# Kernel optimization log

Measured on AMD Instinct MI355X. Metric: run time of the kernel, lower is better.

Reference implementation:

```python
import jax, jax.numpy as jnp
import numpy as np

EMBED = 1024
HEADS = 16
HEAD_DIM = EMBED // HEADS


def setup_inputs() -> dict:
    key = jax.random.key(0)
    k1, k2, k3, k4, k5 = jax.random.split(key, 5)
    N, S = 2, 2048
    values = jax.random.normal(k1, (N, S, EMBED), dtype=jnp.float32)
    keys = jax.random.normal(k2, (N, S, EMBED), dtype=jnp.float32)
    query = jax.random.normal(k3, (N, S, EMBED), dtype=jnp.float32)
    mask = jnp.ones((N, 1, S, S), dtype=jnp.int32)
    # fc_out: Linear(heads*head_dim, embed_size) with bias; torch stores W as [out, in]
    W_out = jax.random.normal(k4, (EMBED, EMBED), dtype=jnp.float32) / np.sqrt(EMBED)
    b_out = jax.random.normal(k5, (EMBED,), dtype=jnp.float32) * 0.01
    return {"values": values, "keys": keys, "query": query, "mask": mask,
            "W_out": W_out, "b_out": b_out}


def reference(values, keys, query, mask, W_out, b_out):
    N, S, E = query.shape
    H, D = HEADS, HEAD_DIM
    # NOTE: source module never applies its q/k/v Linear layers (bug preserved).
    v = values.reshape(N, S, H, D)
    k = keys.reshape(N, S, H, D)
    q = query.reshape(N, S, H, D)
    energy = jnp.einsum('nqhd,nkhd->nhqk', q, k)  # [N,H,S,S]
    energy = jnp.where(mask == 0, jnp.float32(-1e20), energy)
    # non-standard scale: sqrt(embed_size), faithful to source
    attn = jax.nn.softmax(energy / jnp.sqrt(jnp.float32(E)), axis=3)
    out = jnp.einsum('nhql,nlhd->nqhd', attn, v).reshape(N, S, H * D)
    return out @ W_out.T + b_out
```

## Files before the change

### kernel.cpp

```cpp
#include <hip/hip_runtime.h>
#include <stdint.h>

#define S_LEN 2048
#define EMB 1024
#define NHEADS 16
#define HD 64
#define LOG2E 1.4426950408889634f
#define NROWS 65536

typedef __bf16 bf16x8 __attribute__((ext_vector_type(8)));
typedef float f32x4 __attribute__((ext_vector_type(4)));
typedef unsigned short u16;

#define MFMA16(a, b, c) __builtin_amdgcn_mfma_f32_16x16x32_bf16(a, b, c, 0, 0, 0)
#define GLOAD_LDS16(gp, lp)                                        \
  __builtin_amdgcn_global_load_lds(                                \
      (const __attribute__((address_space(1))) unsigned int*)(gp), \
      (__attribute__((address_space(3))) unsigned int*)(lp), 16, 0, 0)

__device__ __forceinline__ u16 bf16r(float x) {
  union { float f; unsigned int u; } c; c.f = x;
  unsigned int u = c.u + 0x7fffu + ((c.u >> 16) & 1u);
  return (u16)(u >> 16);
}

__device__ __forceinline__ unsigned int cvt_pk_bf16(float lo, float hi) {
  unsigned int r;
  asm("v_cvt_pk_bf16_f32 %0, %1, %2" : "=v"(r) : "v"(lo), "v"(hi));
  return r;
}

__device__ __forceinline__ float fexp2(float x) {
  float r;
  asm("v_exp_f32 %0, %1" : "=v"(r) : "v"(x));
  return r;
}

__device__ __forceinline__ float fmax3(float a, float b, float c) {
  float r;
  asm("v_max3_f32 %0, %1, %2, %3" : "=v"(r) : "v"(a), "v"(b), "v"(c));
  return r;
}

__device__ __forceinline__ float bf_lo(unsigned int v) {
  union { unsigned int u; float f; } c; c.u = v << 16; return c.f;
}
__device__ __forceinline__ float bf_hi(unsigned int v) {
  union { unsigned int u; float f; } c; c.u = v & 0xffff0000u; return c.f;
}

__device__ __forceinline__ int kperm(int k) {
  int kb = (k >> 4) & 3, g = (k >> 2) & 3, r = k & 3;
  return (kb >> 1) * 32 + g * 8 + (kb & 1) * 4 + r;
}

__global__ __launch_bounds__(256) void prep_kernel(
    const float* __restrict__ values, const float* __restrict__ keys,
    const float* __restrict__ W, const int* __restrict__ mask,
    u16* __restrict__ vt, u16* __restrict__ kb, u16* __restrict__ wb,
    unsigned char* __restrict__ fl2) {
  __shared__ u16 tile[64][65];
  __shared__ int s_ok[4];
  int b = blockIdx.x;
  int t = threadIdx.x;
  if (b < 1024) {
    int st = b & 31, h = (b >> 5) & 15, n = b >> 9;
    int s0 = st * 64;
    int d = t & 63, r4 = t >> 6;
#pragma unroll
    for (int i = 0; i < 16; ++i) {
      int s = r4 + i * 4;
      float x = values[(size_t)(n * S_LEN + s0 + s) * EMB + h * HD + d];
      tile[s][d] = bf16r(x);
    }
    __syncthreads();
    int sp = s0 + kperm(d);
#pragma unroll
    for (int i = 0; i < 16; ++i) {
      int dd = r4 + i * 4;
      vt[(size_t)((n * NHEADS + h) * HD + dd) * S_LEN + sp] = tile[d][dd];
    }
  } else if (b < 2048) {
    int idx = (b - 1024) * 256 + t;
    const float4* in4 = (const float4*)keys;
    ushort4* out4 = (ushort4*)kb;
#pragma unroll
    for (int j = 0; j < 4; ++j) {
      float4 v = in4[idx + j * 262144];
      ushort4 o;
      o.x = bf16r(v.x); o.y = bf16r(v.y); o.z = bf16r(v.z); o.w = bf16r(v.w);
      out4[idx + j * 262144] = o;
    }
  } else if (b < 2304) {
    int idx = (b - 2048) * 256 + t;
    const float4* in4 = (const float4*)W;
    ushort4* out4 = (ushort4*)wb;
#pragma unroll
    for (int j = 0; j < 4; ++j) {
      float4 v = in4[idx + j * 65536];
      ushort4 o;
      o.x = bf16r(v.x); o.y = bf16r(v.y); o.z = bf16r(v.z); o.w = bf16r(v.w);
      out4[idx + j * 65536] = o;
    }
  } else {
    int idx = b - 2304;
    int kt = idx & 31, qt = (idx >> 5) & 15, n = idx >> 9;
    int qr = t >> 1, c8 = t & 1;
    const int4* mp = (const int4*)(mask + (size_t)n * S_LEN * S_LEN +
                                   (size_t)(qt * 128 + qr) * S_LEN + kt * 64) + c8 * 8;
    int ok = 1;
#pragma unroll
    for (int i = 0; i < 8; ++i) {
      int4 m = mp[i];
      ok &= (m.x != 0) & (m.y != 0) & (m.z != 0) & (m.w != 0);
    }
    ok = __all(ok);
    if ((t & 63) == 0) s_ok[t >> 6] = ok;
    __syncthreads();
    if (t == 0) fl2[idx] = (unsigned char)(s_ok[0] & s_ok[1] & s_ok[2] & s_ok[3]);
  }
}

__global__ __launch_bounds__(256, 4) void attn_kernel(
    const float* __restrict__ query, const u16* __restrict__ kbuf,
    const u16* __restrict__ vt, const int* __restrict__ mask,
    const unsigned char* __restrict__ fl2, u16* __restrict__ po,
    float2* __restrict__ ml) {
  __shared__ __align__(16) unsigned char kl[2][8192];
  __shared__ __align__(16) unsigned char vl[2][8192];

  int b = blockIdx.x;
  b = (b & 7) * 128 + (b >> 3);
  int qt = b & 15, half = (b >> 4) & 1, h = (b >> 5) & 15, n = b >> 9;
  int t = threadIdx.x, w = t >> 6, l = t & 63, l16 = l & 15, g = l >> 4;
  int q0 = qt * 128 + w * 32;
  int kt0 = half * 16;

  const float QS = 0.03125f * LOG2E;
  bf16x8 aq[2][2];
#pragma unroll
  for (int u = 0; u < 2; ++u)
#pragma unroll
    for (int hh = 0; hh < 2; ++hh) {
      const float* qp = query + (size_t)(n * S_LEN + q0 + u * 16 + l16) * EMB +
                        h * HD + hh * 32 + g * 8;
      float4 f0 = *(const float4*)qp;
      float4 f1 = *(const float4*)(qp + 4);
      union { bf16x8 v; unsigned int u32[4]; } qq;
      qq.u32[0] = cvt_pk_bf16(f0.x * QS, f0.y * QS);
      qq.u32[1] = cvt_pk_bf16(f0.z * QS, f0.w * QS);
      qq.u32[2] = cvt_pk_bf16(f1.x * QS, f1.y * QS);
      qq.u32[3] = cvt_pk_bf16(f1.z * QS, f1.w * QS);
      aq[u][hh] = qq.v;
    }

  union { bf16x8 v; unsigned int u32[4]; } one_i;
  one_i.u32[0] = 0x3F803F80u; one_i.u32[1] = 0x3F803F80u;
  one_i.u32[2] = 0x3F803F80u; one_i.u32[3] = 0x3F803F80u;
  bf16x8 ones = one_i.v;

  f32x4 zero4 = {0.f, 0.f, 0.f, 0.f};
  f32x4 acc[2][4];
  float lrun[2] = {0.f, 0.f}, mrun[2] = {0.f, 0.f};
#pragma unroll
  for (int u = 0; u < 2; ++u)
#pragma unroll
    for (int db = 0; db < 4; ++db) acc[u][db] = zero4;

  int row_s = t >> 3, cc = t & 7;
  int sc = cc ^ (row_s & 7);
  const u16* gk0 = kbuf + (size_t)(n * S_LEN + row_s) * EMB + h * HD + sc * 8;
  const u16* gv0 = vt + (size_t)((n * NHEADS + h) * HD + row_s) * S_LEN + sc * 8;

  auto stage = [&](int kt, int nb) {
    const u16* gk = gk0 + (size_t)kt * 64 * EMB;
    const u16* gv = gv0 + kt * 64;
    GLOAD_LDS16(gk, kl[nb] + (w * 64) * 16);
    GLOAD_LDS16(gk + 32 * EMB, kl[nb] + (256 + w * 64) * 16);
    GLOAD_LDS16(gv, vl[nb] + (w * 64) * 16);
    GLOAD_LDS16(gv + 32 * S_LEN, vl[nb] + (256 + w * 64) * 16);
  };

  auto body = [&](int kt, const unsigned char* kc, const unsigned char* vc) {
    f32x4 sf[2][4];
    __builtin_amdgcn_s_setprio(1);
#pragma unroll
    for (int kb = 0; kb < 4; ++kb) {
      int row = kb * 16 + l16;
      const unsigned char* kr = kc + row * 128;
      int sw = (row & 7) << 4;
      bf16x8 bk0 = *(const bf16x8*)(kr + ((g * 16) ^ sw));
      bf16x8 bk1 = *(const bf16x8*)(kr + ((64 + g * 16) ^ sw));
#pragma unroll
      for (int u = 0; u < 2; ++u) {
        f32x4 z = zero4;
        z = MFMA16(bk0, aq[u][0], z);
        z = MFMA16(bk1, aq[u][1], z);
        sf[u][kb] = z;
      }
    }
    __builtin_amdgcn_s_setprio(0);

    unsigned char fflag = fl2[((n * 16 + qt) * 32) + kt];
    if (!fflag) {
#pragma unroll
      for (int u = 0; u < 2; ++u) {
        const int* mrow = mask + (size_t)n * S_LEN * S_LEN +
                          (size_t)(q0 + u * 16 + l16) * S_LEN + kt * 64 + g * 4;
#pragma unroll
        for (int kb = 0; kb < 4; ++kb) {
          int4 mm = *(const int4*)(mrow + kb * 16);
          if (mm.x == 0) sf[u][kb][0] = -100.f;
          if (mm.y == 0) sf[u][kb][1] = -100.f;
          if (mm.z == 0) sf[u][kb][2] = -100.f;
          if (mm.w == 0) sf[u][kb][3] = -100.f;
        }
      }
    }

    bf16x8 pa[2][2];
#pragma unroll
    for (int u = 0; u < 2; ++u) {
      float a0 = fmax3(sf[u][0][0], sf[u][0][1], sf[u][0][2]);
      float a1 = fmax3(sf[u][0][3], sf[u][1][0], sf[u][1][1]);
      float a2 = fmax3(sf[u][1][2], sf[u][1][3], sf[u][2][0]);
      float a3 = fmax3(sf[u][2][1], sf[u][2][2], sf[u][2][3]);
      float a4 = fmax3(sf[u][3][0], sf[u][3][1], sf[u][3][2]);
      float lmax = fmaxf(fmax3(a0, a1, a2), fmax3(a3, a4, sf[u][3][3]));
      if (!__all(lmax <= mrun[u] + 8.f)) {
        float rmax = fmaxf(lmax, __shfl_xor(lmax, 16));
        rmax = fmaxf(rmax, __shfl_xor(rmax, 32));
        float Mn = fmaxf(mrun[u], rmax);
        float corr = fexp2(mrun[u] - Mn);
        mrun[u] = Mn;
        lrun[u] *= corr;
#pragma unroll
        for (int r = 0; r < 4; ++r) {
          float ca = __shfl(corr, (l & 48) + (g << 2) + r);
#pragma unroll
          for (int db = 0; db < 4; ++db) acc[u][db][r] *= ca;
        }
      }
      float p[4][4];
      if (__all(mrun[u] == 0.f)) {
#pragma unroll
        for (int kb = 0; kb < 4; ++kb)
#pragma unroll
          for (int r = 0; r < 4; ++r) p[kb][r] = fexp2(sf[u][kb][r]);
      } else {
#pragma unroll
        for (int kb = 0; kb < 4; ++kb)
#pragma unroll
          for (int r = 0; r < 4; ++r) p[kb][r] = fexp2(sf[u][kb][r] - mrun[u]);
      }
#pragma unroll
      for (int hh = 0; hh < 2; ++hh) {
        union { bf16x8 v; unsigned int u32[4]; } pp;
        pp.u32[0] = cvt_pk_bf16(p[2 * hh][0], p[2 * hh][1]);
        pp.u32[1] = cvt_pk_bf16(p[2 * hh][2], p[2 * hh][3]);
        pp.u32[2] = cvt_pk_bf16(p[2 * hh + 1][0], p[2 * hh + 1][1]);
        pp.u32[3] = cvt_pk_bf16(p[2 * hh + 1][2], p[2 * hh + 1][3]);
        pa[u][hh] = pp.v;
      }
      f32x4 z = zero4;
      z = MFMA16(pa[u][0], ones, z);
      z = MFMA16(pa[u][1], ones, z);
      float z01 = (l16 & 1) ? z[1] : z[0];
      float z23 = (l16 & 1) ? z[3] : z[2];
      float zsel = (l16 & 2) ? z23 : z01;
      lrun[u] += __shfl(zsel, ((l16 >> 2) << 4) + (l16 & 3));
    }

    __builtin_amdgcn_s_setprio(1);
#pragma unroll
    for (int hh = 0; hh < 2; ++hh)
#pragma unroll
      for (int db = 0; db < 4; ++db) {
        int d = db * 16 + l16;
        bf16x8 bv = *(const bf16x8*)(vc + d * 128 + ((hh * 64 + g * 16) ^ ((d & 7) << 4)));
        acc[0][db] = MFMA16(pa[0][hh], bv, acc[0][db]);
        acc[1][db] = MFMA16(pa[1][hh], bv, acc[1][db]);
      }
    __builtin_amdgcn_s_setprio(0);
  };

  stage(kt0, 0);
  __syncthreads();

#pragma unroll 1
  for (int kt = kt0; kt < kt0 + 16; kt += 2) {
    stage(kt + 1, 1);
    body(kt, kl[0], vl[0]);
    __syncthreads();
    if (kt + 2 < kt0 + 16) stage(kt + 2, 0);
    body(kt + 1, kl[1], vl[1]);
    __syncthreads();
  }

  size_t rowbase = (size_t)(n * NHEADS + h) * S_LEN + q0;
#pragma unroll
  for (int u = 0; u < 2; ++u) {
    if (g == 0) {
      float2 v; v.x = mrun[u]; v.y = lrun[u];
      ml[(size_t)half * NROWS + rowbase + u * 16 + l16] = v;
    }
#pragma unroll
    for (int db = 0; db < 4; ++db)
#pragma unroll
      for (int r = 0; r < 4; ++r) {
        size_t rq = rowbase + u * 16 + (g << 2) + r;
        po[((size_t)half * NROWS + rq) * HD + db * 16 + l16] = bf16r(acc[u][db][r]);
      }
  }
}

__global__ __launch_bounds__(256) void combine_kernel(
    const u16* __restrict__ po, const float2* __restrict__ ml,
    u16* __restrict__ ob) {
  int idx = blockIdx.x * 256 + threadIdx.x;
  int row = idx >> 3, d8 = idx & 7;
  float2 a = ml[row], b = ml[NROWS + row];
  float m = fmaxf(a.x, b.x);
  float c0 = fexp2(a.x - m), c1 = fexp2(b.x - m);
  float rinv = 1.f / (a.y * c0 + b.y * c1);
  c0 *= rinv; c1 *= rinv;
  uint4 p0 = *(const uint4*)(po + (size_t)row * HD + d8 * 8);
  uint4 p1 = *(const uint4*)(po + ((size_t)NROWS + row) * HD + d8 * 8);
  uint4 o;
  o.x = cvt_pk_bf16(bf_lo(p0.x) * c0 + bf_lo(p1.x) * c1,
                    bf_hi(p0.x) * c0 + bf_hi(p1.x) * c1);
  o.y = cvt_pk_bf16(bf_lo(p0.y) * c0 + bf_lo(p1.y) * c1,
                    bf_hi(p0.y) * c0 + bf_hi(p1.y) * c1);
  o.z = cvt_pk_bf16(bf_lo(p0.z) * c0 + bf_lo(p1.z) * c1,
                    bf_hi(p0.z) * c0 + bf_hi(p1.z) * c1);
  o.w = cvt_pk_bf16(bf_lo(p0.w) * c0 + bf_lo(p1.w) * c1,
                    bf_hi(p0.w) * c0 + bf_hi(p1.w) * c1);
  int n = row >> 15, h = (row >> 11) & 15, q = row & 2047;
  *(uint4*)(ob + (size_t)(n * S_LEN + q) * EMB + h * HD + d8 * 8) = o;
}

__global__ __launch_bounds__(256, 3) void proj_kernel(
    const u16* __restrict__ A, const u16* __restrict__ Bt,
    const float* __restrict__ bias, float* __restrict__ C) {
  __shared__ __align__(16) unsigned char al[2][16384];
  __shared__ __align__(16) unsigned char bl[2][8192];
  int bm = blockIdx.x, bn = blockIdx.y;
  int t = threadIdx.x, w = t >> 6, l = t & 63;
  int l16 = l & 15, g = l >> 4;
  f32x4 zero4 = {0.f, 0.f, 0.f, 0.f};
  f32x4 acc[2][4];
#pragma unroll
  for (int mi = 0; mi < 2; ++mi)
#pragma unroll
    for (int nj = 0; nj < 4; ++nj) acc[mi][nj] = zero4;
  int row_s = t >> 3, cc = t & 7;
  int sc = cc ^ (row_s & 7);
  const u16* ga0 = A + (size_t)(bm * 128 + row_s) * EMB + sc * 8;
  const u16* gb0 = Bt + (size_t)(bn * 64 + row_s) * EMB + sc * 8;

  auto stage = [&](int ks, int nb) {
#pragma unroll
    for (int i = 0; i < 4; ++i)
      GLOAD_LDS16(ga0 + (size_t)i * 32 * EMB + ks * 64, al[nb] + (i * 256 + w * 64) * 16);
#pragma unroll
    for (int i = 0; i < 2; ++i)
      GLOAD_LDS16(gb0 + (size_t)i * 32 * EMB + ks * 64, bl[nb] + (i * 256 + w * 64) * 16);
  };

  auto body = [&](const unsigned char* ac, const unsigned char* bc) {
    __builtin_amdgcn_s_setprio(1);
#pragma unroll
    for (int hh = 0; hh < 2; ++hh) {
      bf16x8 af[2], bfr[4];
#pragma unroll
      for (int mi = 0; mi < 2; ++mi) {
        int row = w * 32 + mi * 16 + l16;
        af[mi] = *(const bf16x8*)(ac + row * 128 + ((hh * 64 + g * 16) ^ ((row & 7) << 4)));
      }
#pragma unroll
      for (int nj = 0; nj < 4; ++nj) {
        int row = nj * 16 + l16;
        bfr[nj] = *(const bf16x8*)(bc + row * 128 + ((hh * 64 + g * 16) ^ ((row & 7) << 4)));
      }
#pragma unroll
      for (int mi = 0; mi < 2; ++mi)
#pragma unroll
        for (int nj = 0; nj < 4; ++nj) acc[mi][nj] = MFMA16(af[mi], bfr[nj], acc[mi][nj]);
    }
    __builtin_amdgcn_s_setprio(0);
  };

  stage(0, 0);
  __syncthreads();

#pragma unroll 1
  for (int ks = 0; ks < 16; ks += 2) {
    stage(ks + 1, 1);
    body(al[0], bl[0]);
    __syncthreads();
    if (ks + 2 < 16) stage(ks + 2, 0);
    body(al[1], bl[1]);
    __syncthreads();
  }
#pragma unroll
  for (int nj = 0; nj < 4; ++nj) {
    int j = bn * 64 + nj * 16 + l16;
    float bj = bias[j];
#pragma unroll
    for (int mi = 0; mi < 2; ++mi) {
      int i0 = bm * 128 + w * 32 + mi * 16 + g * 4;
#pragma unroll
      for (int r = 0; r < 4; ++r) C[(size_t)(i0 + r) * EMB + j] = acc[mi][nj][r] + bj;
    }
  }
}

extern "C" void kernel_launch(void* const* d_in, const int* in_sizes, int n_in,
                              void* d_out, int out_size, void* d_ws, size_t ws_size,
                              hipStream_t stream) {
  const float* values = (const float*)d_in[0];
  const float* keys = (const float*)d_in[1];
  const float* query = (const float*)d_in[2];
  const int* mask = (const int*)d_in[3];
  const float* W = (const float*)d_in[4];
  const float* bias = (const float*)d_in[5];
  float* out = (float*)d_out;

  u16* kb = (u16*)d_ws;
  u16* vt = kb + 4194304;
  u16* ob = vt + 4194304;
  u16* wb = ob + 4194304;
  unsigned char* fl2 = (unsigned char*)(wb + 1048576);
  u16* po = (u16*)(fl2 + 65536);
  float2* ml = (float2*)(po + 2 * (size_t)NROWS * HD);

  prep_kernel<<<3328, 256, 0, stream>>>(values, keys, W, mask, vt, kb, wb, fl2);
  attn_kernel<<<1024, 256, 0, stream>>>(query, kb, vt, mask, fl2, po, ml);
  combine_kernel<<<2048, 256, 0, stream>>>(po, ml, ob);
  proj_kernel<<<dim3(32, 16), 256, 0, stream>>>(ob, wb, bias, out);
}
```

Before: 87.58 us.

## Split attention key range into four chunks and combine four partials

Each attention block now covers a quarter of the key sequence instead of half, which doubles the grid to 2048 blocks. The combine kernel merges four partial softmax results instead of two. The launch-bounds occupancy hint goes from 4 to 5 blocks per CU. The aim is more parallelism and better latency hiding across the CUs, at the cost of doubled partial-output traffic, extra per-block Q load and setup, and more register pressure from the tighter occupancy target.

Measured after the change: 173.7 us. 1.98x slower.

```diff
diff --git a/kernel.cpp b/kernel.cpp
--- a/kernel.cpp
+++ b/kernel.cpp
@@ -121,7 +121,7 @@
   }
 }
 
-__global__ __launch_bounds__(256, 4) void attn_kernel(
+__global__ __launch_bounds__(256, 5) void attn_kernel(
     const float* __restrict__ query, const u16* __restrict__ kbuf,
     const u16* __restrict__ vt, const int* __restrict__ mask,
     const unsigned char* __restrict__ fl2, u16* __restrict__ po,
@@ -130,11 +130,11 @@
   __shared__ __align__(16) unsigned char vl[2][8192];
 
   int b = blockIdx.x;
-  b = (b & 7) * 128 + (b >> 3);
-  int qt = b & 15, half = (b >> 4) & 1, h = (b >> 5) & 15, n = b >> 9;
+  b = (b & 7) * 256 + (b >> 3);
+  int qt = b & 15, half = (b >> 4) & 3, h = (b >> 6) & 15, n = b >> 10;
   int t = threadIdx.x, w = t >> 6, l = t & 63, l16 = l & 15, g = l >> 4;
   int q0 = qt * 128 + w * 32;
-  int kt0 = half * 16;
+  int kt0 = half * 8;
 
   const float QS = 0.03125f * LOG2E;
   bf16x8 aq[2][2];
@@ -288,11 +288,11 @@
   __syncthreads();
 
 #pragma unroll 1
-  for (int kt = kt0; kt < kt0 + 16; kt += 2) {
+  for (int kt = kt0; kt < kt0 + 8; kt += 2) {
     stage(kt + 1, 1);
     body(kt, kl[0], vl[0]);
     __syncthreads();
-    if (kt + 2 < kt0 + 16) stage(kt + 2, 0);
+    if (kt + 2 < kt0 + 8) stage(kt + 2, 0);
     body(kt + 1, kl[1], vl[1]);
     __syncthreads();
   }
@@ -319,22 +319,30 @@
     u16* __restrict__ ob) {
   int idx = blockIdx.x * 256 + threadIdx.x;
   int row = idx >> 3, d8 = idx & 7;
-  float2 a = ml[row], b = ml[NROWS + row];
-  float m = fmaxf(a.x, b.x);
-  float c0 = fexp2(a.x - m), c1 = fexp2(b.x - m);
-  float rinv = 1.f / (a.y * c0 + b.y * c1);
-  c0 *= rinv; c1 *= rinv;
+  float2 a0 = ml[row], a1 = ml[NROWS + row];
+  float2 a2 = ml[2 * (size_t)NROWS + row], a3 = ml[3 * (size_t)NROWS + row];
+  float m = fmaxf(fmaxf(a0.x, a1.x), fmaxf(a2.x, a3.x));
+  float c0 = fexp2(a0.x - m), c1 = fexp2(a1.x - m);
+  float c2 = fexp2(a2.x - m), c3 = fexp2(a3.x - m);
+  float rinv = 1.f / (a0.y * c0 + a1.y * c1 + a2.y * c2 + a3.y * c3);
+  c0 *= rinv; c1 *= rinv; c2 *= rinv; c3 *= rinv;
   uint4 p0 = *(const uint4*)(po + (size_t)row * HD + d8 * 8);
   uint4 p1 = *(const uint4*)(po + ((size_t)NROWS + row) * HD + d8 * 8);
+  uint4 p2 = *(const uint4*)(po + (2 * (size_t)NROWS + row) * HD + d8 * 8);
+  uint4 p3 = *(const uint4*)(po + (3 * (size_t)NROWS + row) * HD + d8 * 8);
   uint4 o;
-  o.x = cvt_pk_bf16(bf_lo(p0.x) * c0 + bf_lo(p1.x) * c1,
-                    bf_hi(p0.x) * c0 + bf_hi(p1.x) * c1);
-  o.y = cvt_pk_bf16(bf_lo(p0.y) * c0 + bf_lo(p1.y) * c1,
-                    bf_hi(p0.y) * c0 + bf_hi(p1.y) * c1);
-  o.z = cvt_pk_bf16(bf_lo(p0.z) * c0 + bf_lo(p1.z) * c1,
-                    bf_hi(p0.z) * c0 + bf_hi(p1.z) * c1);
-  o.w = cvt_pk_bf16(bf_lo(p0.w) * c0 + bf_lo(p1.w) * c1,
-                    bf_hi(p0.w) * c0 + bf_hi(p1.w) * c1);
+  o.x = cvt_pk_bf16(
+      bf_lo(p0.x) * c0 + bf_lo(p1.x) * c1 + bf_lo(p2.x) * c2 + bf_lo(p3.x) * c3,
+      bf_hi(p0.x) * c0 + bf_hi(p1.x) * c1 + bf_hi(p2.x) * c2 + bf_hi(p3.x) * c3);
+  o.y = cvt_pk_bf16(
+      bf_lo(p0.y) * c0 + bf_lo(p1.y) * c1 + bf_lo(p2.y) * c2 + bf_lo(p3.y) * c3,
+      bf_hi(p0.y) * c0 + bf_hi(p1.y) * c1 + bf_hi(p2.y) * c2 + bf_hi(p3.y) * c3);
+  o.z = cvt_pk_bf16(
+      bf_lo(p0.z) * c0 + bf_lo(p1.z) * c1 + bf_lo(p2.z) * c2 + bf_lo(p3.z) * c3,
+      bf_hi(p0.z) * c0 + bf_hi(p1.z) * c1 + bf_hi(p2.z) * c2 + bf_hi(p3.z) * c3);
+  o.w = cvt_pk_bf16(
+      bf_lo(p0.w) * c0 + bf_lo(p1.w) * c1 + bf_lo(p2.w) * c2 + bf_lo(p3.w) * c3,
+      bf_hi(p0.w) * c0 + bf_hi(p1.w) * c1 + bf_hi(p2.w) * c2 + bf_hi(p3.w) * c3);
   int n = row >> 15, h = (row >> 11) & 15, q = row & 2047;
   *(uint4*)(ob + (size_t)(n * S_LEN + q) * EMB + h * HD + d8 * 8) = o;
 }
@@ -432,10 +440,10 @@
   u16* wb = ob + 4194304;
   unsigned char* fl2 = (unsigned char*)(wb + 1048576);
   u16* po = (u16*)(fl2 + 65536);
-  float2* ml = (float2*)(po + 2 * (size_t)NROWS * HD);
+  float2* ml = (float2*)(po + 4 * (size_t)NROWS * HD);
 
   prep_kernel<<<3328, 256, 0, stream>>>(values, keys, W, mask, vt, kb, wb, fl2);
-  attn_kernel<<<1024, 256, 0, stream>>>(query, kb, vt, mask, fl2, po, ml);
+  attn_kernel<<<2048, 256, 0, stream>>>(query, kb, vt, mask, fl2, po, ml);
   combine_kernel<<<2048, 256, 0, stream>>>(po, ml, ob);
   proj_kernel<<<dim3(32, 16), 256, 0, stream>>>(ob, wb, bias, out);
 }
```
